# Kernel optimization log

Measured on AMD Instinct MI355X. Metric: run time of the kernel, lower is better.

## Reference

```python
import jax, jax.numpy as jnp
import numpy as np
from jax import lax

BITS = 8
CLIP = 2.0 ** (BITS - 1) - 1.0  # 127 for int8 symmetric quantization
EPS = 1e-6


def _quantize(x):
    """Dynamic per-tensor symmetric quantization (AQT-style).

    Returns the integer-valued (but float-dtype) quantized tensor and the
    scale such that dequant = q / scale.
    """
    bound = jnp.maximum(jnp.max(jnp.abs(x)), EPS)
    scale = CLIP / bound
    q = jnp.clip(jnp.round(x * scale), -CLIP, CLIP)
    return q, scale


def setup_inputs() -> dict:
    key = jax.random.key(0)
    k1, k2 = jax.random.split(key)
    lhs = jax.random.normal(k1, (4096, 4096), dtype=jnp.float32)
    rhs = jax.random.normal(k2, (4096, 4096), dtype=jnp.float32)
    return {"lhs": lhs, "rhs": rhs}


def reference(lhs, rhs):
    # Quantize both operands with dynamically computed per-tensor scales,
    # do the matmul on the integer-valued tensors, then dequantize the
    # result by the product of scales. This is the math aqt_ops.aqt_dot
    q_lhs, s_lhs = _quantize(lhs)
    q_rhs, s_rhs = _quantize(rhs)
    acc = jnp.matmul(q_lhs, q_rhs)  # [M, N], integer-valued accumulation
    return acc / (s_lhs * s_rhs)
```

## Files before the change

kernel.cpp:

```cpp
#include <hip/hip_runtime.h>
#include <hip/hip_bf16.h>


typedef int v4i __attribute__((ext_vector_type(4)));

#define MAT_N 4096

__device__ __forceinline__ void async_copy16(const void* g, void* l) {
    __builtin_amdgcn_global_load_lds(
        (const __attribute__((address_space(1))) void*)g,
        (__attribute__((address_space(3))) void*)l,
        16, 0, 0);
}

__global__ __launch_bounds__(256) void absmax_kernel(
    const float4* __restrict__ x, int n4, unsigned* __restrict__ slot) {
    unsigned m = 0u;
    for (int i = blockIdx.x * blockDim.x + threadIdx.x; i < n4;
         i += blockDim.x * gridDim.x) {
        float4 v = x[i];
        unsigned a = __float_as_uint(v.x) & 0x7fffffffu;
        unsigned b = __float_as_uint(v.y) & 0x7fffffffu;
        unsigned c = __float_as_uint(v.z) & 0x7fffffffu;
        unsigned d = __float_as_uint(v.w) & 0x7fffffffu;
        m = max(m, max(max(a, b), max(c, d)));
    }
#pragma unroll
    for (int off = 32; off > 0; off >>= 1)
        m = max(m, (unsigned)__shfl_down(m, off, 64));
    __shared__ unsigned sm[4];
    if ((threadIdx.x & 63) == 0) sm[threadIdx.x >> 6] = m;
    __syncthreads();
    if (threadIdx.x == 0) {
        m = max(max(sm[0], sm[1]), max(sm[2], sm[3]));
        atomicMax(slot, m);
    }
}

__global__ __launch_bounds__(256) void quant_kernel(
    const float* __restrict__ x, unsigned char* __restrict__ q,
    const unsigned* __restrict__ slot) {
    const float s = 127.0f / fmaxf(__uint_as_float(*slot), 1e-6f);
    const float4* x4 = (const float4*)x;
    unsigned* q4 = (unsigned*)q;
    const int base4 = blockIdx.x * 1024;
#pragma unroll
    for (int u = 0; u < 4; u++) {
        int idx = base4 + u * 256 + threadIdx.x;
        float4 v = x4[idx];
        int a = min(127, max(-127, (int)rintf(v.x * s)));
        int b = min(127, max(-127, (int)rintf(v.y * s)));
        int c = min(127, max(-127, (int)rintf(v.z * s)));
        int d = min(127, max(-127, (int)rintf(v.w * s)));
        q4[idx] = (unsigned)(a & 0xff) | ((unsigned)(b & 0xff) << 8) |
                  ((unsigned)(c & 0xff) << 16) | ((unsigned)(d & 0xff) << 24);
    }
}

__global__ __launch_bounds__(256) void quantT_kernel(
    const float* __restrict__ x, signed char* __restrict__ qT,
    const unsigned* __restrict__ slot) {
    const int N = MAT_N;
    const float s = 127.0f / fmaxf(__uint_as_float(*slot), 1e-6f);
    __shared__ signed char sm[64][68];
    const int k0 = blockIdx.y * 64, n0 = blockIdx.x * 64;
    const int t = threadIdx.x;
    const int n = t & 63, kb = t >> 6;
#pragma unroll
    for (int r = 0; r < 16; r++) {
        int k = r * 4 + kb;
        float v = x[(size_t)(k0 + k) * N + n0 + n];
        int qi = min(127, max(-127, (int)rintf(v * s)));
        sm[k][n] = (signed char)qi;
    }
    __syncthreads();
    const int nn = t >> 2, cb = (t & 3) * 16;
    union { signed char b[16]; int4 v; } tmp;
#pragma unroll
    for (int i = 0; i < 16; i++) tmp.b[i] = sm[cb + i][nn];
    *(int4*)(qT + (size_t)(n0 + nn) * N + k0 + cb) = tmp.v;
}

__global__ __launch_bounds__(256) void gemm_i8_kernel(
    const signed char* __restrict__ A, const signed char* __restrict__ BT,
    float* __restrict__ C, const unsigned* __restrict__ slots) {
    const int N = MAT_N;
    __shared__ __align__(16) signed char As[128 * 64];
    __shared__ __align__(16) signed char Bs[128 * 64];

    const int tid = threadIdx.x;
    const int wave = tid >> 6;
    const int lane = tid & 63;
    const int quad = lane >> 4;
    const int mrow = lane & 15;
    const int wr = (wave >> 1) * 64;
    const int wc = (wave & 1) * 64;
    const int brow = blockIdx.y * 128;
    const int bcol = blockIdx.x * 128;

    v4i acc[4][4] = {};

    const int c0 = wave * 64 + lane;
    const size_t aoff0 = (size_t)(brow + (c0 >> 2)) * N + (c0 & 3) * 16;
    const size_t aoff1 = aoff0 + (size_t)64 * N;
    const size_t boff0 = (size_t)(bcol + (c0 >> 2)) * N + (c0 & 3) * 16;
    const size_t boff1 = boff0 + (size_t)64 * N;
    signed char* a_l0 = As + c0 * 16;
    signed char* a_l1 = As + (c0 + 256) * 16;
    signed char* b_l0 = Bs + c0 * 16;
    signed char* b_l1 = Bs + (c0 + 256) * 16;

    for (int k0 = 0; k0 < N; k0 += 64) {
        __syncthreads();
        async_copy16(A + aoff0 + k0, a_l0);
        async_copy16(A + aoff1 + k0, a_l1);
        async_copy16(BT + boff0 + k0, b_l0);
        async_copy16(BT + boff1 + k0, b_l1);
        __syncthreads();

        const v4i* Av = (const v4i*)As;
        const v4i* Bv = (const v4i*)Bs;
        v4i af[4], bf[4];
#pragma unroll
        for (int i = 0; i < 4; i++) af[i] = Av[(wr + i * 16 + mrow) * 4 + quad];
#pragma unroll
        for (int j = 0; j < 4; j++) bf[j] = Bv[(wc + j * 16 + mrow) * 4 + quad];
#pragma unroll
        for (int i = 0; i < 4; i++)
#pragma unroll
            for (int j = 0; j < 4; j++)
                acc[i][j] = __builtin_amdgcn_mfma_i32_16x16x64_i8(
                    af[i], bf[j], acc[i][j], 0, 0, 0);
    }

    const float bl = fmaxf(__uint_as_float(slots[0]), 1e-6f);
    const float br = fmaxf(__uint_as_float(slots[1]), 1e-6f);
    const float dq = bl * br * (1.0f / (127.0f * 127.0f));

#pragma unroll
    for (int i = 0; i < 4; i++) {
        const int row0 = brow + wr + i * 16 + quad * 4;
#pragma unroll
        for (int j = 0; j < 4; j++) {
            const int col = bcol + wc + j * 16 + mrow;
#pragma unroll
            for (int r = 0; r < 4; r++)
                C[(size_t)(row0 + r) * N + col] = (float)acc[i][j][r] * dq;
        }
    }
}

extern "C" void kernel_launch(void* const* d_in, const int* in_sizes, int n_in,
                              void* d_out, int out_size, void* d_ws, size_t ws_size,
                              hipStream_t stream) {
    const float* lhs = (const float*)d_in[0];
    const float* rhs = (const float*)d_in[1];
    float* out = (float*)d_out;

    unsigned* slots = (unsigned*)d_ws;
    signed char* qA = (signed char*)d_ws + 256;
    signed char* qBT = qA + (size_t)MAT_N * MAT_N;

    const int n4 = MAT_N * MAT_N / 4;

    hipMemsetAsync(d_ws, 0, 8, stream);
    absmax_kernel<<<2048, 256, 0, stream>>>((const float4*)lhs, n4, slots + 0);
    absmax_kernel<<<2048, 256, 0, stream>>>((const float4*)rhs, n4, slots + 1);
    quant_kernel<<<MAT_N * MAT_N / 4096, 256, 0, stream>>>(
        lhs, (unsigned char*)qA, slots + 0);
    quantT_kernel<<<dim3(64, 64), 256, 0, stream>>>(rhs, qBT, slots + 1);
    gemm_i8_kernel<<<dim3(32, 32), 256, 0, stream>>>(qA, qBT, out, slots);
}
```

Before: 316.3 us.

## Merge absmax and quant launches, use float4 transpose, deepen GEMM K-tile with swizzle

The two absmax launches become one kernel over both inputs, with four independent max chains per thread. The two quantize kernels become one fused launch, and the transposed path now reads float4 and shuffles bytes with perm instructions instead of doing byte-wise shared-memory transposes. The int8 GEMM doubles its K tile to 128, halving the number of barrier pairs, and XOR-swizzles the LDS layout to avoid bank conflicts on fragment loads. LDS use per block rises to 32KB, which may reduce occupancy, and loads are still not overlapped with compute.

After: 278.1 us. 12.1% less time.

```diff
diff --git a/kernel.cpp b/kernel.cpp
--- a/kernel.cpp
+++ b/kernel.cpp
@@ -13,18 +13,28 @@
         16, 0, 0);
 }
 
-__global__ __launch_bounds__(256) void absmax_kernel(
-    const float4* __restrict__ x, int n4, unsigned* __restrict__ slot) {
-    unsigned m = 0u;
-    for (int i = blockIdx.x * blockDim.x + threadIdx.x; i < n4;
-         i += blockDim.x * gridDim.x) {
+__device__ __forceinline__ unsigned uabs_bits(float f) {
+    return __float_as_uint(f) & 0x7fffffffu;
+}
+
+__global__ __launch_bounds__(256) void absmax2_kernel(
+    const float4* __restrict__ lhs, const float4* __restrict__ rhs,
+    unsigned* __restrict__ slots) {
+    const float4* x = lhs;
+    unsigned* slot = slots;
+    int b = blockIdx.x;
+    if (b >= 2048) { x = rhs; slot = slots + 1; b -= 2048; }
+    unsigned m0 = 0, m1 = 0, m2 = 0, m3 = 0;
+    int i = b * 256 + threadIdx.x;
+#pragma unroll
+    for (int u = 0; u < 8; u++, i += 524288) {
         float4 v = x[i];
-        unsigned a = __float_as_uint(v.x) & 0x7fffffffu;
-        unsigned b = __float_as_uint(v.y) & 0x7fffffffu;
-        unsigned c = __float_as_uint(v.z) & 0x7fffffffu;
-        unsigned d = __float_as_uint(v.w) & 0x7fffffffu;
-        m = max(m, max(max(a, b), max(c, d)));
-    }
+        m0 = max(m0, uabs_bits(v.x));
+        m1 = max(m1, uabs_bits(v.y));
+        m2 = max(m2, uabs_bits(v.z));
+        m3 = max(m3, uabs_bits(v.w));
+    }
+    unsigned m = max(max(m0, m1), max(m2, m3));
 #pragma unroll
     for (int off = 32; off > 0; off >>= 1)
         m = max(m, (unsigned)__shfl_down(m, off, 64));
@@ -37,56 +47,74 @@
     }
 }
 
-__global__ __launch_bounds__(256) void quant_kernel(
-    const float* __restrict__ x, unsigned char* __restrict__ q,
-    const unsigned* __restrict__ slot) {
-    const float s = 127.0f / fmaxf(__uint_as_float(*slot), 1e-6f);
-    const float4* x4 = (const float4*)x;
-    unsigned* q4 = (unsigned*)q;
-    const int base4 = blockIdx.x * 1024;
-#pragma unroll
-    for (int u = 0; u < 4; u++) {
-        int idx = base4 + u * 256 + threadIdx.x;
-        float4 v = x4[idx];
-        int a = min(127, max(-127, (int)rintf(v.x * s)));
-        int b = min(127, max(-127, (int)rintf(v.y * s)));
-        int c = min(127, max(-127, (int)rintf(v.z * s)));
-        int d = min(127, max(-127, (int)rintf(v.w * s)));
-        q4[idx] = (unsigned)(a & 0xff) | ((unsigned)(b & 0xff) << 8) |
-                  ((unsigned)(c & 0xff) << 16) | ((unsigned)(d & 0xff) << 24);
-    }
-}
-
-__global__ __launch_bounds__(256) void quantT_kernel(
-    const float* __restrict__ x, signed char* __restrict__ qT,
-    const unsigned* __restrict__ slot) {
+__global__ __launch_bounds__(256) void quant_fused_kernel(
+    const float* __restrict__ lhs, const float* __restrict__ rhs,
+    unsigned char* __restrict__ qA, signed char* __restrict__ qBT,
+    const unsigned* __restrict__ slots) {
     const int N = MAT_N;
-    const float s = 127.0f / fmaxf(__uint_as_float(*slot), 1e-6f);
-    __shared__ signed char sm[64][68];
-    const int k0 = blockIdx.y * 64, n0 = blockIdx.x * 64;
     const int t = threadIdx.x;
-    const int n = t & 63, kb = t >> 6;
-#pragma unroll
-    for (int r = 0; r < 16; r++) {
-        int k = r * 4 + kb;
-        float v = x[(size_t)(k0 + k) * N + n0 + n];
-        int qi = min(127, max(-127, (int)rintf(v * s)));
-        sm[k][n] = (signed char)qi;
-    }
-    __syncthreads();
-    const int nn = t >> 2, cb = (t & 3) * 16;
-    union { signed char b[16]; int4 v; } tmp;
-#pragma unroll
-    for (int i = 0; i < 16; i++) tmp.b[i] = sm[cb + i][nn];
-    *(int4*)(qT + (size_t)(n0 + nn) * N + k0 + cb) = tmp.v;
+    __shared__ __align__(16) signed char smT[64 * 80];
+
+    int b = blockIdx.x;
+    if (b < 4096) {
+        const float s = 127.0f / fmaxf(__uint_as_float(slots[0]), 1e-6f);
+        const float4* x4 = (const float4*)lhs;
+        unsigned* q4 = (unsigned*)qA;
+        const int base4 = b * 1024;
+#pragma unroll
+        for (int u = 0; u < 4; u++) {
+            int idx = base4 + u * 256 + t;
+            float4 v = x4[idx];
+            int a = min(127, max(-127, (int)rintf(v.x * s)));
+            int bq = min(127, max(-127, (int)rintf(v.y * s)));
+            int c = min(127, max(-127, (int)rintf(v.z * s)));
+            int d = min(127, max(-127, (int)rintf(v.w * s)));
+            q4[idx] = (unsigned)(a & 0xff) | ((unsigned)(bq & 0xff) << 8) |
+                      ((unsigned)(c & 0xff) << 16) | ((unsigned)(d & 0xff) << 24);
+        }
+    } else {
+        const float s = 127.0f / fmaxf(__uint_as_float(slots[1]), 1e-6f);
+        b -= 4096;
+        const int n0 = (b & 63) * 64;
+        const int k0 = (b >> 6) * 64;
+        const int mk = t >> 4;
+        const int mn = t & 15;
+        const float4* x4 = (const float4*)rhs;
+
+        unsigned w[4];
+#pragma unroll
+        for (int i = 0; i < 4; i++) {
+            float4 v = x4[(size_t)(k0 + 4 * mk + i) * (N / 4) + (n0 >> 2) + mn];
+            int a = min(127, max(-127, (int)rintf(v.x * s)));
+            int bq = min(127, max(-127, (int)rintf(v.y * s)));
+            int c = min(127, max(-127, (int)rintf(v.z * s)));
+            int d = min(127, max(-127, (int)rintf(v.w * s)));
+            w[i] = (unsigned)(a & 0xff) | ((unsigned)(bq & 0xff) << 8) |
+                   ((unsigned)(c & 0xff) << 16) | ((unsigned)(d & 0xff) << 24);
+        }
+#pragma unroll
+        for (int j = 0; j < 4; j++) {
+            unsigned selj = (unsigned)j | ((unsigned)(4 + j) << 8) |
+                            ((unsigned)j << 16) | ((unsigned)(4 + j) << 24);
+            unsigned p01 = __builtin_amdgcn_perm(w[1], w[0], selj);
+            unsigned p23 = __builtin_amdgcn_perm(w[3], w[2], selj);
+            unsigned uj = __builtin_amdgcn_perm(p23, p01, 0x05040100u);
+            *(unsigned*)(smT + (4 * mn + j) * 80 + 4 * mk) = uj;
+        }
+        __syncthreads();
+        const int nr = t >> 2;
+        const int kq = (t & 3) * 16;
+        int4 val = *(const int4*)(smT + nr * 80 + kq);
+        *(int4*)(qBT + (size_t)(n0 + nr) * N + k0 + kq) = val;
+    }
 }
 
 __global__ __launch_bounds__(256) void gemm_i8_kernel(
     const signed char* __restrict__ A, const signed char* __restrict__ BT,
     float* __restrict__ C, const unsigned* __restrict__ slots) {
     const int N = MAT_N;
-    __shared__ __align__(16) signed char As[128 * 64];
-    __shared__ __align__(16) signed char Bs[128 * 64];
+    __shared__ __align__(16) signed char As[128 * 128];
+    __shared__ __align__(16) signed char Bs[128 * 128];
 
     const int tid = threadIdx.x;
     const int wave = tid >> 6;
@@ -100,37 +128,49 @@
 
     v4i acc[4][4] = {};
 
-    const int c0 = wave * 64 + lane;
-    const size_t aoff0 = (size_t)(brow + (c0 >> 2)) * N + (c0 & 3) * 16;
-    const size_t aoff1 = aoff0 + (size_t)64 * N;
-    const size_t boff0 = (size_t)(bcol + (c0 >> 2)) * N + (c0 & 3) * 16;
-    const size_t boff1 = boff0 + (size_t)64 * N;
-    signed char* a_l0 = As + c0 * 16;
-    signed char* a_l1 = As + (c0 + 256) * 16;
-    signed char* b_l0 = Bs + c0 * 16;
-    signed char* b_l1 = Bs + (c0 + 256) * 16;
-
-    for (int k0 = 0; k0 < N; k0 += 64) {
+    int gaoff[4], gboff[4];
+    signed char* la[4];
+    signed char* lb[4];
+#pragma unroll
+    for (int u = 0; u < 4; u++) {
+        int c = tid + 256 * u;
+        int r = c >> 3;
+        int q = (c & 7) ^ (r & 7);
+        gaoff[u] = (brow + r) * N + q * 16;
+        gboff[u] = (bcol + r) * N + q * 16;
+        la[u] = As + c * 16;
+        lb[u] = Bs + c * 16;
+    }
+
+    for (int k0 = 0; k0 < N; k0 += 128) {
         __syncthreads();
-        async_copy16(A + aoff0 + k0, a_l0);
-        async_copy16(A + aoff1 + k0, a_l1);
-        async_copy16(BT + boff0 + k0, b_l0);
-        async_copy16(BT + boff1 + k0, b_l1);
+#pragma unroll
+        for (int u = 0; u < 4; u++) async_copy16(A + gaoff[u] + k0, la[u]);
+#pragma unroll
+        for (int u = 0; u < 4; u++) async_copy16(BT + gboff[u] + k0, lb[u]);
         __syncthreads();
 
-        const v4i* Av = (const v4i*)As;
-        const v4i* Bv = (const v4i*)Bs;
-        v4i af[4], bf[4];
-#pragma unroll
-        for (int i = 0; i < 4; i++) af[i] = Av[(wr + i * 16 + mrow) * 4 + quad];
-#pragma unroll
-        for (int j = 0; j < 4; j++) bf[j] = Bv[(wc + j * 16 + mrow) * 4 + quad];
-#pragma unroll
-        for (int i = 0; i < 4; i++)
-#pragma unroll
-            for (int j = 0; j < 4; j++)
-                acc[i][j] = __builtin_amdgcn_mfma_i32_16x16x64_i8(
-                    af[i], bf[j], acc[i][j], 0, 0, 0);
+#pragma unroll
+        for (int s = 0; s < 2; s++) {
+            const int kq = s * 4 + quad;
+            v4i af[4], bf[4];
+#pragma unroll
+            for (int i = 0; i < 4; i++) {
+                int r = wr + i * 16 + mrow;
+                af[i] = *(const v4i*)(As + (r * 8 + (kq ^ (r & 7))) * 16);
+            }
+#pragma unroll
+            for (int j = 0; j < 4; j++) {
+                int r = wc + j * 16 + mrow;
+                bf[j] = *(const v4i*)(Bs + (r * 8 + (kq ^ (r & 7))) * 16);
+            }
+#pragma unroll
+            for (int i = 0; i < 4; i++)
+#pragma unroll
+                for (int j = 0; j < 4; j++)
+                    acc[i][j] = __builtin_amdgcn_mfma_i32_16x16x64_i8(
+                        af[i], bf[j], acc[i][j], 0, 0, 0);
+        }
     }
 
     const float bl = fmaxf(__uint_as_float(slots[0]), 1e-6f);
@@ -161,13 +201,10 @@
     signed char* qA = (signed char*)d_ws + 256;
     signed char* qBT = qA + (size_t)MAT_N * MAT_N;
 
-    const int n4 = MAT_N * MAT_N / 4;
-
     hipMemsetAsync(d_ws, 0, 8, stream);
-    absmax_kernel<<<2048, 256, 0, stream>>>((const float4*)lhs, n4, slots + 0);
-    absmax_kernel<<<2048, 256, 0, stream>>>((const float4*)rhs, n4, slots + 1);
-    quant_kernel<<<MAT_N * MAT_N / 4096, 256, 0, stream>>>(
-        lhs, (unsigned char*)qA, slots + 0);
-    quantT_kernel<<<dim3(64, 64), 256, 0, stream>>>(rhs, qBT, slots + 1);
+    absmax2_kernel<<<4096, 256, 0, stream>>>(
+        (const float4*)lhs, (const float4*)rhs, slots);
+    quant_fused_kernel<<<8192, 256, 0, stream>>>(
+        lhs, rhs, (unsigned char*)qA, qBT, slots);
     gemm_i8_kernel<<<dim3(32, 32), 256, 0, stream>>>(qA, qBT, out, slots);
 }
```
